# Kernel optimization log

Measured on AMD Instinct MI355X. Metric: run time of the kernel, lower is better.

The kernel has to match this reference:

```python
import jax, jax.numpy as jnp
import numpy as np

N = 32
R = 128  # num_regions
F = 128  # num_features


def setup_inputs() -> dict:
    key = jax.random.key(0)
    k1, k2, k3, k4 = jax.random.split(key, 4)
    x1 = jax.random.normal(k1, (N, R * F), dtype=jnp.float32)
    x2 = jax.random.normal(k2, (N, R * F), dtype=jnp.float32)
    sigma = jax.random.normal(k3, (1,), dtype=jnp.float32) * 100.0
    mean = jax.random.normal(k4, (1,), dtype=jnp.float32)
    return {"x1": x1, "x2": x2, "sigma": sigma, "mean": mean}


def reference(x1, x2, sigma, mean):
    # (N, R, 1, F) - (N, 1, R, F) - mean -> (N, R, R, F)
    a = x1.reshape(N, R, 1, F)
    b = x2.reshape(N, 1, R, F)
    diff = a - b - mean  # mean is shape (1,), broadcasts over F
    distance_squared = jnp.sum(diff * diff, axis=-1)  # (N, R, R)
    kernel_value = jnp.exp(-distance_squared / (2.0 * sigma[0] ** 2))
    return jax.nn.softmax(kernel_value, axis=-1)
```

## Files before the change

### kernel.cpp

```cpp
#include <hip/hip_runtime.h>

#define NB 32
#define RR 128
#define FF 128

__global__ __launch_bounds__(256) void transpose_x2(const float* __restrict__ x2,
                                                    float* __restrict__ x2t) {
  __shared__ float tile[32][33];
  const int n = blockIdx.z;
  const int jt = blockIdx.x * 32;
  const int ft = blockIdx.y * 32;
  const int tx = threadIdx.x;
  const int ty = threadIdx.y;
  const float* src = x2 + (size_t)n * RR * FF;
  float* dst = x2t + (size_t)n * RR * FF;
#pragma unroll
  for (int k = 0; k < 32; k += 8)
    tile[ty + k][tx] = src[(jt + ty + k) * FF + ft + tx];
  __syncthreads();
#pragma unroll
  for (int k = 0; k < 32; k += 8)
    dst[(ft + ty + k) * RR + jt + tx] = tile[tx][ty + k];
}

template <bool TRANSPOSED>
__global__ __launch_bounds__(128) void gauss_softmax(const float* __restrict__ x1,
                                                     const float* __restrict__ xb,
                                                     const float* __restrict__ sigma,
                                                     const float* __restrict__ mean,
                                                     float* __restrict__ out) {
  const int bid = blockIdx.x;
  const int n = bid >> 5;
  const int i0 = (bid & 31) << 2;
  const int tid = threadIdx.x;
  const int tx = tid & 31;
  const int ty = tid >> 5;
  __shared__ float sh_a[4 * FF];

  const float mval = mean[0];
  const float sg = sigma[0];
  const float cneg = -1.0f / (2.0f * sg * sg);

  {
    const float4 v = ((const float4*)(x1 + (size_t)(n * RR + i0) * FF))[tid];
    ((float4*)sh_a)[tid] = make_float4(v.x - mval, v.y - mval, v.z - mval, v.w - mval);
  }
  __syncthreads();

  float acc0 = 0.f, acc1 = 0.f, acc2 = 0.f, acc3 = 0.f;
  const float* base = xb + (size_t)n * RR * FF;
  const int j0 = tx << 2;
  const float* arow = sh_a + ty * FF;

#pragma unroll 8
  for (int f = 0; f < FF; ++f) {
    float4 b;
    if (TRANSPOSED) {
      b = *(const float4*)(base + f * RR + j0);
    } else {
      b.x = base[(j0 + 0) * FF + f];
      b.y = base[(j0 + 1) * FF + f];
      b.z = base[(j0 + 2) * FF + f];
      b.w = base[(j0 + 3) * FF + f];
    }
    const float a = arow[f];
    float d;
    d = a - b.x; acc0 = fmaf(d, d, acc0);
    d = a - b.y; acc1 = fmaf(d, d, acc1);
    d = a - b.z; acc2 = fmaf(d, d, acc2);
    d = a - b.w; acc3 = fmaf(d, d, acc3);
  }

  const float k0 = __expf(acc0 * cneg);
  const float k1 = __expf(acc1 * cneg);
  const float k2 = __expf(acc2 * cneg);
  const float k3 = __expf(acc3 * cneg);

  float mx = fmaxf(fmaxf(k0, k1), fmaxf(k2, k3));
#pragma unroll
  for (int off = 16; off >= 1; off >>= 1) mx = fmaxf(mx, __shfl_xor(mx, off, 64));
  const float e0 = __expf(k0 - mx);
  const float e1 = __expf(k1 - mx);
  const float e2 = __expf(k2 - mx);
  const float e3 = __expf(k3 - mx);
  float ssum = e0 + e1 + e2 + e3;
#pragma unroll
  for (int off = 16; off >= 1; off >>= 1) ssum += __shfl_xor(ssum, off, 64);
  const float r = 1.0f / ssum;

  *(float4*)(out + (size_t)(n * RR + i0 + ty) * RR + j0) =
      make_float4(e0 * r, e1 * r, e2 * r, e3 * r);
}

extern "C" void kernel_launch(void* const* d_in, const int* in_sizes, int n_in,
                              void* d_out, int out_size, void* d_ws, size_t ws_size,
                              hipStream_t stream) {
  const float* x1 = (const float*)d_in[0];
  const float* x2 = (const float*)d_in[1];
  const float* sigma = (const float*)d_in[2];
  const float* mean = (const float*)d_in[3];
  float* out = (float*)d_out;

  const size_t needed = (size_t)NB * RR * FF * sizeof(float);
  if (ws_size >= needed) {
    float* x2t = (float*)d_ws;
    transpose_x2<<<dim3(4, 4, NB), dim3(32, 8), 0, stream>>>(x2, x2t);
    gauss_softmax<true><<<dim3(NB * 32), dim3(128), 0, stream>>>(x1, x2t, sigma, mean, out);
  } else {
    gauss_softmax<false><<<dim3(NB * 32), dim3(128), 0, stream>>>(x1, x2, sigma, mean, out);
  }
}
```

Baseline: 72.10 us.

## Fuse x2 transpose into main kernel via shared-memory tiling

Removes the separate transpose kernel and workspace round trip. Each block now handles 8 rows of x1 against one batch's x2, loading 32-feature slabs of x2 into padded shared memory in transposed form before accumulating distances. Block size grows to 256 threads and the grid halves. This saves one launch and a global write/read of x2, at the cost of more syncthreads and strided shared-memory stores.

```diff
diff --git a/kernel.cpp b/kernel.cpp
--- a/kernel.cpp
+++ b/kernel.cpp
@@ -3,39 +3,23 @@
 #define NB 32
 #define RR 128
 #define FF 128
+#define FT 32
+#define SB 132
 
-__global__ __launch_bounds__(256) void transpose_x2(const float* __restrict__ x2,
-                                                    float* __restrict__ x2t) {
-  __shared__ float tile[32][33];
-  const int n = blockIdx.z;
-  const int jt = blockIdx.x * 32;
-  const int ft = blockIdx.y * 32;
-  const int tx = threadIdx.x;
-  const int ty = threadIdx.y;
-  const float* src = x2 + (size_t)n * RR * FF;
-  float* dst = x2t + (size_t)n * RR * FF;
-#pragma unroll
-  for (int k = 0; k < 32; k += 8)
-    tile[ty + k][tx] = src[(jt + ty + k) * FF + ft + tx];
-  __syncthreads();
-#pragma unroll
-  for (int k = 0; k < 32; k += 8)
-    dst[(ft + ty + k) * RR + jt + tx] = tile[tx][ty + k];
-}
+__global__ __launch_bounds__(256) void gauss_fused(const float* __restrict__ x1,
+                                                   const float* __restrict__ x2,
+                                                   const float* __restrict__ sigma,
+                                                   const float* __restrict__ mean,
+                                                   float* __restrict__ out) {
+  __shared__ __align__(16) float sh_b[FT * SB];
+  __shared__ __align__(16) float sh_a[8 * FF];
 
-template <bool TRANSPOSED>
-__global__ __launch_bounds__(128) void gauss_softmax(const float* __restrict__ x1,
-                                                     const float* __restrict__ xb,
-                                                     const float* __restrict__ sigma,
-                                                     const float* __restrict__ mean,
-                                                     float* __restrict__ out) {
   const int bid = blockIdx.x;
-  const int n = bid >> 5;
-  const int i0 = (bid & 31) << 2;
+  const int n = bid >> 4;
+  const int i0 = (bid & 15) << 3;
   const int tid = threadIdx.x;
   const int tx = tid & 31;
   const int ty = tid >> 5;
-  __shared__ float sh_a[4 * FF];
 
   const float mval = mean[0];
   const float sg = sigma[0];
@@ -45,30 +29,39 @@
     const float4 v = ((const float4*)(x1 + (size_t)(n * RR + i0) * FF))[tid];
     ((float4*)sh_a)[tid] = make_float4(v.x - mval, v.y - mval, v.z - mval, v.w - mval);
   }
-  __syncthreads();
+
+  const float* __restrict__ x2base = x2 + (size_t)n * RR * FF;
+  const int jj = tid >> 3;
+  const int fo = (tid & 7) << 2;
 
   float acc0 = 0.f, acc1 = 0.f, acc2 = 0.f, acc3 = 0.f;
-  const float* base = xb + (size_t)n * RR * FF;
   const int j0 = tx << 2;
-  const float* arow = sh_a + ty * FF;
+  const float* __restrict__ arow = sh_a + ty * FF;
 
-#pragma unroll 8
-  for (int f = 0; f < FF; ++f) {
-    float4 b;
-    if (TRANSPOSED) {
-      b = *(const float4*)(base + f * RR + j0);
-    } else {
-      b.x = base[(j0 + 0) * FF + f];
-      b.y = base[(j0 + 1) * FF + f];
-      b.z = base[(j0 + 2) * FF + f];
-      b.w = base[(j0 + 3) * FF + f];
+  for (int t = 0; t < FF / FT; ++t) {
+    const int ftw = t * FT;
+    __syncthreads();
+#pragma unroll
+    for (int p = 0; p < 4; ++p) {
+      const int j = jj + p * 32;
+      const float4 v = *(const float4*)(x2base + (size_t)j * FF + ftw + fo);
+      sh_b[(fo + 0) * SB + j] = v.x;
+      sh_b[(fo + 1) * SB + j] = v.y;
+      sh_b[(fo + 2) * SB + j] = v.z;
+      sh_b[(fo + 3) * SB + j] = v.w;
     }
-    const float a = arow[f];
-    float d;
-    d = a - b.x; acc0 = fmaf(d, d, acc0);
-    d = a - b.y; acc1 = fmaf(d, d, acc1);
-    d = a - b.z; acc2 = fmaf(d, d, acc2);
-    d = a - b.w; acc3 = fmaf(d, d, acc3);
+    __syncthreads();
+
+#pragma unroll
+    for (int f = 0; f < FT; ++f) {
+      const float4 b = *(const float4*)(sh_b + f * SB + j0);
+      const float a = arow[ftw + f];
+      float d;
+      d = a - b.x; acc0 = fmaf(d, d, acc0);
+      d = a - b.y; acc1 = fmaf(d, d, acc1);
+      d = a - b.z; acc2 = fmaf(d, d, acc2);
+      d = a - b.w; acc3 = fmaf(d, d, acc3);
+    }
   }
 
   const float k0 = __expf(acc0 * cneg);
@@ -100,13 +93,7 @@
   const float* sigma = (const float*)d_in[2];
   const float* mean = (const float*)d_in[3];
   float* out = (float*)d_out;
+  (void)d_ws; (void)ws_size;
 
-  const size_t needed = (size_t)NB * RR * FF * sizeof(float);
-  if (ws_size >= needed) {
-    float* x2t = (float*)d_ws;
-    transpose_x2<<<dim3(4, 4, NB), dim3(32, 8), 0, stream>>>(x2, x2t);
-    gauss_softmax<true><<<dim3(NB * 32), dim3(128), 0, stream>>>(x1, x2t, sigma, mean, out);
-  } else {
-    gauss_softmax<false><<<dim3(NB * 32), dim3(128), 0, stream>>>(x1, x2, sigma, mean, out);
-  }
+  gauss_fused<<<dim3(NB * 16), dim3(256), 0, stream>>>(x1, x2, sigma, mean, out);
 }
```

After: 69.07 us. -4.2%, faster.
